# Kernel optimization log

Hardware: AMD Instinct MI355X
Metric: run time of the kernel (lower is better)

Reference implementation:

```python
import jax, jax.numpy as jnp
import numpy as np

N_NODES = 100000
N_EDGES = 1600000
H = 128
NUM_INV = 16
BN_EPS = 1e-5


def setup_inputs() -> dict:
    key = jax.random.key(0)
    ks = jax.random.split(key, 12)
    x_send = jax.random.normal(ks[0], (N_NODES, H), dtype=jnp.float32)
    x_rec = jax.random.normal(ks[1], (N_NODES, H), dtype=jnp.float32)
    index_send = jax.random.randint(ks[2], (N_EDGES,), 0, N_NODES, dtype=jnp.int32)
    index_rec = jax.random.randint(ks[3], (N_EDGES,), 0, N_NODES, dtype=jnp.int32)
    edge_attr = jax.random.normal(ks[4], (N_EDGES, NUM_INV), dtype=jnp.float32)
    d_in = 2 * H + NUM_INV
    # Linear(2H+num_inv -> H), BatchNorm1d(H) affine, Linear(H -> 1)
    W1 = jax.random.normal(ks[5], (d_in, H), dtype=jnp.float32) / np.sqrt(d_in)
    b1 = jnp.zeros((H,), dtype=jnp.float32)
    gamma = jnp.ones((H,), dtype=jnp.float32)
    beta = jnp.zeros((H,), dtype=jnp.float32)
    W_inf = jax.random.normal(ks[6], (H, 1), dtype=jnp.float32) / np.sqrt(H)
    b_inf = jnp.zeros((1,), dtype=jnp.float32)
    return {
        "x_send": x_send, "x_rec": x_rec,
        "index_send": index_send, "index_rec": index_rec,
        "edge_attr": edge_attr,
        "W1": W1, "b1": b1, "gamma": gamma, "beta": beta,
        "W_inf": W_inf, "b_inf": b_inf,
    }


def reference(x_send, x_rec, index_send, index_rec, edge_attr, W1, b1, gamma, beta, W_inf, b_inf):
    # gather sender/receiver features per edge: [E, H]
    sim_send = x_send[index_send]
    sim_rec = x_rec[index_rec]
    state = jnp.concatenate((sim_send, sim_rec, edge_attr), axis=1)  # [E, 2H+inv]
    h = state @ W1 + b1  # [E, H]
    # BatchNorm1d (training mode): batch statistics over edge dim, biased var
    mean = jnp.mean(h, axis=0)
    var = jnp.mean(jnp.square(h - mean), axis=0)
    h = (h - mean) * jax.lax.rsqrt(var + BN_EPS) * gamma + beta
    messages = jax.nn.silu(h)  # [E, H]
    edge_weights = jax.nn.sigmoid(messages @ W_inf + b_inf)  # [E, 1]
    # scatter_add over receiver index
    messages_aggr = jax.ops.segment_sum(messages * edge_weights, index_rec, num_segments=x_rec.shape[0])
    return messages_aggr
```

## Files before the change

### kernel.cpp

```cpp
#include <hip/hip_runtime.h>
#include <hip/hip_bf16.h>

#define N_NODES 100000
#define N_EDGES 1600000
#define H 128
#define NUM_INV 16
#define BN_EPS 1e-5f

typedef __attribute__((ext_vector_type(8))) short short8;
typedef __attribute__((ext_vector_type(4))) float f32x4;
typedef __attribute__((ext_vector_type(2))) float f32x2;

static __device__ __forceinline__ unsigned short f2b(float x) {
    union { float f; unsigned u; } c; c.f = x;
    unsigned r = c.u + 0x7fffu + ((c.u >> 16) & 1u);
    return (unsigned short)(r >> 16);
}
static __device__ __forceinline__ f32x2 b2f2(unsigned u) {
    union { unsigned u; float f; } lo, hi;
    lo.u = u << 16;
    hi.u = u & 0xffff0000u;
    return (f32x2){lo.f, hi.f};
}
static __device__ __forceinline__ unsigned pack2(f32x2 v) {
    return (unsigned)f2b(v.x) | ((unsigned)f2b(v.y) << 16);
}
static __device__ __forceinline__ f32x2 splat2(float s) { return (f32x2){s, s}; }

template<int CTRL, int RM>
static __device__ __forceinline__ float dppadd(float x) {
    union { float f; int i; } u, s;
    u.f = x;
    s.i = __builtin_amdgcn_update_dpp(0, u.i, CTRL, RM, 0xf, true);
    return x + s.f;
}
static __device__ __forceinline__ float wave_sum_bcast(float p) {
    p = dppadd<0x111, 0xf>(p);
    p = dppadd<0x112, 0xf>(p);
    p = dppadd<0x114, 0xf>(p);
    p = dppadd<0x118, 0xf>(p);
    p = dppadd<0x142, 0xa>(p);
    p = dppadd<0x143, 0xc>(p);
    union { float f; int i; } u, r;
    u.f = p;
    r.i = __builtin_amdgcn_readlane(u.i, 63);
    return r.f;
}

static __device__ __forceinline__ f32x2 ea_mac(const float* __restrict__ ea, int e,
                                               const f32x2* wc2, f32x2 h2) {
    const f32x4* ep = (const f32x4*)(ea + (size_t)e * NUM_INV);
    f32x4 e0 = ep[0], e1 = ep[1], e2 = ep[2], e3 = ep[3];
    float ev[16] = {e0[0],e0[1],e0[2],e0[3], e1[0],e1[1],e1[2],e1[3],
                    e2[0],e2[1],e2[2],e2[3], e3[0],e3[1],e3[2],e3[3]};
    #pragma unroll
    for (int k = 0; k < NUM_INV; ++k) h2 += splat2(ev[k]) * wc2[k];
    return h2;
}

static __device__ __forceinline__ f32x2 ea_mac_b16(const unsigned short* __restrict__ eab,
                                                   int slot, const f32x2* wc2, f32x2 h2) {
    const uint4* p = (const uint4*)(eab + (size_t)slot * NUM_INV);
    uint4 w0 = p[0], w1 = p[1];
    unsigned wv[8] = {w0.x, w0.y, w0.z, w0.w, w1.x, w1.y, w1.z, w1.w};
    #pragma unroll
    for (int k = 0; k < 8; ++k) {
        f32x2 ev = b2f2(wv[k]);
        h2 += splat2(ev.x) * wc2[2 * k] + splat2(ev.y) * wc2[2 * k + 1];
    }
    return h2;
}

__global__ void k0_wt(const float* __restrict__ W1, unsigned short* __restrict__ Wt) {
    int idx = blockIdx.x * blockDim.x + threadIdx.x;
    if (idx >= 2 * H * H) return;
    int g = idx >> 14;
    int rem = idx & 16383;
    int k = rem >> 7;
    int f = rem & 127;
    Wt[(size_t)g * H * H + (size_t)f * H + k] = f2b(W1[(size_t)(g * H + k) * H + f]);
}

__global__ __launch_bounds__(256) void k1_gemm(
    const float* __restrict__ x_send, const float* __restrict__ x_rec,
    const unsigned short* __restrict__ Wt, const float* __restrict__ b1,
    unsigned short* __restrict__ P_send, unsigned short* __restrict__ P_rec)
{
    const int g = blockIdx.y;
    const float* X = g ? x_rec : x_send;
    unsigned short* P = g ? P_rec : P_send;
    const int m0 = blockIdx.x * 32;
    const int tid = threadIdx.x;
    const int wave = tid >> 6;
    const int lane = tid & 63;
    const int quad = lane >> 4;
    const int l16 = lane & 15;
    const int n0 = wave * 32;

    const unsigned short* Wg = Wt + (size_t)g * (H * H);

    f32x4 acc[2][2];
    #pragma unroll
    for (int i = 0; i < 2; ++i)
        #pragma unroll
        for (int j = 0; j < 2; ++j)
            acc[i][j] = (f32x4){0.f, 0.f, 0.f, 0.f};

    #pragma unroll
    for (int kt = 0; kt < 4; ++kt) {
        const int kk = kt * 32;
        short8 a[2], b[2];
        #pragma unroll
        for (int ms = 0; ms < 2; ++ms) {
            const float* ap = X + (size_t)(m0 + ms * 16 + l16) * H + kk + quad * 8;
            f32x4 a0 = *(const f32x4*)ap;
            f32x4 a1 = *(const f32x4*)(ap + 4);
            short8 t;
            t[0] = (short)f2b(a0[0]); t[1] = (short)f2b(a0[1]);
            t[2] = (short)f2b(a0[2]); t[3] = (short)f2b(a0[3]);
            t[4] = (short)f2b(a1[0]); t[5] = (short)f2b(a1[1]);
            t[6] = (short)f2b(a1[2]); t[7] = (short)f2b(a1[3]);
            a[ms] = t;
        }
        #pragma unroll
        for (int ns = 0; ns < 2; ++ns)
            b[ns] = *(const short8*)(Wg + (size_t)(n0 + ns * 16 + l16) * H + kk + quad * 8);
        #pragma unroll
        for (int ms = 0; ms < 2; ++ms)
            #pragma unroll
            for (int ns = 0; ns < 2; ++ns)
                acc[ms][ns] = __builtin_amdgcn_mfma_f32_16x16x32_bf16(
                    a[ms], b[ns], acc[ms][ns], 0, 0, 0);
    }

    #pragma unroll
    for (int ms = 0; ms < 2; ++ms) {
        #pragma unroll
        for (int ns = 0; ns < 2; ++ns) {
            int col = n0 + ns * 16 + l16;
            float bias = g ? 0.f : b1[col];
            #pragma unroll
            for (int r = 0; r < 4; ++r) {
                int row = m0 + ms * 16 + quad * 4 + r;
                P[(size_t)row * H + col] = f2b(acc[ms][ns][r] + bias);
            }
        }
    }
}

__global__ void k_deg(const int* __restrict__ irec, int* __restrict__ deg) {
    int e = blockIdx.x * 256 + threadIdx.x;
    if (e < N_EDGES) atomicAdd(&deg[irec[e]], 1);
}

__global__ __launch_bounds__(512) void k_scanA(const int* __restrict__ deg, int* __restrict__ bsum) {
    __shared__ int sh[512];
    int t = threadIdx.x;
    int n = blockIdx.x * 512 + t;
    int v = (n < N_NODES) ? deg[n] : 0;
    sh[t] = v; __syncthreads();
    for (int d = 1; d < 512; d <<= 1) {
        int x = (t >= d) ? sh[t - d] : 0;
        __syncthreads();
        sh[t] += x;
        __syncthreads();
    }
    if (t == 511) bsum[blockIdx.x] = sh[511];
}

__global__ __launch_bounds__(256) void k_scanB(const int* __restrict__ bsum, int* __restrict__ bbase) {
    __shared__ int sh[256];
    int t = threadIdx.x;
    int v = (t < 196) ? bsum[t] : 0;
    sh[t] = v; __syncthreads();
    for (int d = 1; d < 256; d <<= 1) {
        int x = (t >= d) ? sh[t - d] : 0;
        __syncthreads();
        sh[t] += x;
        __syncthreads();
    }
    if (t < 196) bbase[t] = sh[t] - v;
}

__global__ __launch_bounds__(512) void k_scanC(const int* __restrict__ deg, const int* __restrict__ bbase,
                                               int* __restrict__ off, int* __restrict__ cursor) {
    __shared__ int sh[512];
    int t = threadIdx.x;
    int n = blockIdx.x * 512 + t;
    int v = (n < N_NODES) ? deg[n] : 0;
    sh[t] = v; __syncthreads();
    for (int d = 1; d < 512; d <<= 1) {
        int x = (t >= d) ? sh[t - d] : 0;
        __syncthreads();
        sh[t] += x;
        __syncthreads();
    }
    if (n < N_NODES) {
        int o = bbase[blockIdx.x] + sh[t] - v;
        off[n] = o;
        cursor[n] = o;
    }
}

__global__ void k_perm(const int* __restrict__ irec, const int* __restrict__ isend,
                       int* __restrict__ cursor,
                       int* __restrict__ perm, int* __restrict__ is_csr) {
    int e = blockIdx.x * 256 + threadIdx.x;
    if (e >= N_EDGES) return;
    int p = atomicAdd(&cursor[irec[e]], 1);
    perm[p] = e;
    is_csr[p] = isend[e];
}

__global__ __launch_bounds__(256) void k_permEA(const int* __restrict__ perm,
                                                const float* __restrict__ ea,
                                                unsigned short* __restrict__ eab)
{
    int p = blockIdx.x * 256 + threadIdx.x;
    if (p >= N_EDGES) return;
    int e = perm[p];
    const f32x4* ep = (const f32x4*)(ea + (size_t)e * NUM_INV);
    f32x4 a = ep[0], b = ep[1], c = ep[2], d = ep[3];
    unsigned o0 = pack2((f32x2){a[0], a[1]});
    unsigned o1 = pack2((f32x2){a[2], a[3]});
    unsigned o2 = pack2((f32x2){b[0], b[1]});
    unsigned o3 = pack2((f32x2){b[2], b[3]});
    unsigned o4 = pack2((f32x2){c[0], c[1]});
    unsigned o5 = pack2((f32x2){c[2], c[3]});
    unsigned o6 = pack2((f32x2){d[0], d[1]});
    unsigned o7 = pack2((f32x2){d[2], d[3]});
    uint4* op = (uint4*)(eab + (size_t)p * NUM_INV);
    op[0] = make_uint4(o0, o1, o2, o3);
    op[1] = make_uint4(o4, o5, o6, o7);
}

template<int MODE>
__global__ __launch_bounds__(256) void k2_csr(
    const unsigned short* __restrict__ Ps, const unsigned short* __restrict__ Pr,
    const int* __restrict__ is_csr, const int* __restrict__ perm,
    const float* __restrict__ ea, const unsigned short* __restrict__ eab,
    const float* __restrict__ W1,
    const int* __restrict__ off, const int* __restrict__ deg,
    float* __restrict__ stats)
{
    const int tid = threadIdx.x;
    const int wave = tid >> 6;
    const int lane = tid & 63;
    const int f0 = lane * 2;
    const float* Wc = W1 + 2 * H * H;

    f32x2 wc2[NUM_INV];
    #pragma unroll
    for (int k = 0; k < NUM_INV; ++k)
        wc2[k] = (f32x2){Wc[k * H + f0], Wc[k * H + f0 + 1]};

    int n = blockIdx.x * 4 + wave;
    int nu = __builtin_amdgcn_readfirstlane(n);
    int start = off[nu];
    int d = deg[nu];

    f32x2 pr2 = b2f2(*(const unsigned*)(Pr + (size_t)nu * H + f0));

    f32x2 s2 = {0.f, 0.f}, q2 = {0.f, 0.f};
    int i = 0;
    for (; i + 2 <= d; i += 2) {
        int is0 = __builtin_amdgcn_readfirstlane(is_csr[start + i]);
        int is1 = __builtin_amdgcn_readfirstlane(is_csr[start + i + 1]);
        unsigned ua0 = *(const unsigned*)(Ps + (size_t)is0 * H + f0);
        unsigned ua1 = *(const unsigned*)(Ps + (size_t)is1 * H + f0);
        f32x2 h0 = pr2 + b2f2(ua0);
        f32x2 h1 = pr2 + b2f2(ua1);
        if (MODE == 0) {
            h0 = ea_mac_b16(eab, start + i, wc2, h0);
            h1 = ea_mac_b16(eab, start + i + 1, wc2, h1);
        } else {
            int e0 = __builtin_amdgcn_readfirstlane(perm[start + i]);
            int e1 = __builtin_amdgcn_readfirstlane(perm[start + i + 1]);
            h0 = ea_mac(ea, e0, wc2, h0);
            h1 = ea_mac(ea, e1, wc2, h1);
        }
        s2 += h0 + h1;
        q2 += h0 * h0 + h1 * h1;
    }
    if (i < d) {
        int is0 = __builtin_amdgcn_readfirstlane(is_csr[start + i]);
        unsigned ua0 = *(const unsigned*)(Ps + (size_t)is0 * H + f0);
        f32x2 h0 = pr2 + b2f2(ua0);
        if (MODE == 0) {
            h0 = ea_mac_b16(eab, start + i, wc2, h0);
        } else {
            int e0 = __builtin_amdgcn_readfirstlane(perm[start + i]);
            h0 = ea_mac(ea, e0, wc2, h0);
        }
        s2 += h0;
        q2 += h0 * h0;
    }

    __shared__ float rs[4][128];
    __shared__ float rq[4][128];
    rs[wave][f0] = s2.x; rs[wave][f0 + 1] = s2.y;
    rq[wave][f0] = q2.x; rq[wave][f0 + 1] = q2.y;
    __syncthreads();
    if (tid < 128) {
        float ss = rs[0][tid] + rs[1][tid] + rs[2][tid] + rs[3][tid];
        float qq = rq[0][tid] + rq[1][tid] + rq[2][tid] + rq[3][tid];
        float* st = stats + (size_t)(blockIdx.x & 63) * 256;
        atomicAdd(st + tid, ss);
        atomicAdd(st + 128 + tid, qq);
    }
}

__global__ void k3_finalize(const float* __restrict__ stats,
                            const float* __restrict__ gamma, const float* __restrict__ beta,
                            float* __restrict__ ssb)
{
    int f = threadIdx.x;
    if (f >= H) return;
    float s = 0.f, q = 0.f;
    for (int b = 0; b < 64; ++b) {
        s += stats[b * 256 + f];
        q += stats[b * 256 + 128 + f];
    }
    const float invE = 1.f / (float)N_EDGES;
    float mean = s * invE;
    float var = q * invE - mean * mean;
    float scale = gamma[f] * rsqrtf(var + BN_EPS);
    ssb[f] = scale;
    ssb[H + f] = beta[f] - mean * scale;
}

__global__ __launch_bounds__(256) void k4_csr(
    const unsigned short* __restrict__ Ps, const unsigned short* __restrict__ Pr,
    const int* __restrict__ perm, const int* __restrict__ is_csr,
    const float* __restrict__ ea, const float* __restrict__ W1,
    const int* __restrict__ off, const int* __restrict__ deg,
    const float* __restrict__ ssb, const float* __restrict__ Winf,
    const float* __restrict__ binf_p, float* __restrict__ out)
{
    const int tid = threadIdx.x;
    const int wave = tid >> 6;
    const int lane = tid & 63;
    const int f0 = lane * 2;
    const float* Wc = W1 + 2 * H * H;

    f32x2 wc2[NUM_INV];
    #pragma unroll
    for (int k = 0; k < NUM_INV; ++k)
        wc2[k] = (f32x2){Wc[k * H + f0], Wc[k * H + f0 + 1]};

    int n = blockIdx.x * 4 + wave;
    int nu = __builtin_amdgcn_readfirstlane(n);
    int start = off[nu];
    int d = deg[nu];

    unsigned ub = *(const unsigned*)(Pr + (size_t)nu * H + f0);
    f32x2 pr2 = b2f2(ub);

    f32x2 sc2 = (f32x2){ssb[f0], ssb[f0 + 1]};
    f32x2 sh2 = (f32x2){ssb[H + f0], ssb[H + f0 + 1]};
    f32x2 wi2 = (f32x2){Winf[f0], Winf[f0 + 1]};
    float bi = binf_p[0];

    f32x2 a2 = {0.f, 0.f};
    int i = 0;
    for (; i + 2 <= d; i += 2) {
        int e0 = __builtin_amdgcn_readfirstlane(perm[start + i]);
        int e1 = __builtin_amdgcn_readfirstlane(perm[start + i + 1]);
        int is0 = __builtin_amdgcn_readfirstlane(is_csr[start + i]);
        int is1 = __builtin_amdgcn_readfirstlane(is_csr[start + i + 1]);
        unsigned ua0 = *(const unsigned*)(Ps + (size_t)is0 * H + f0);
        unsigned ua1 = *(const unsigned*)(Ps + (size_t)is1 * H + f0);
        f32x2 h0 = ea_mac(ea, e0, wc2, pr2 + b2f2(ua0));
        f32x2 h1 = ea_mac(ea, e1, wc2, pr2 + b2f2(ua1));
        h0 = h0 * sc2 + sh2;
        h1 = h1 * sc2 + sh2;
        float A0 = 1.f + __expf(-h0.x), B0 = 1.f + __expf(-h0.y);
        float A1 = 1.f + __expf(-h1.x), B1 = 1.f + __expf(-h1.y);
        float r0 = __builtin_amdgcn_rcpf(A0 * B0);
        float r1 = __builtin_amdgcn_rcpf(A1 * B1);
        f32x2 m0 = (f32x2){h0.x * B0 * r0, h0.y * A0 * r0};
        f32x2 m1 = (f32x2){h1.x * B1 * r1, h1.y * A1 * r1};
        f32x2 pp0 = m0 * wi2;
        f32x2 pp1 = m1 * wi2;
        float pt0 = wave_sum_bcast(pp0.x + pp0.y);
        float pt1 = wave_sum_bcast(pp1.x + pp1.y);
        float ew0 = __builtin_amdgcn_rcpf(1.f + __expf(-(pt0 + bi)));
        float ew1 = __builtin_amdgcn_rcpf(1.f + __expf(-(pt1 + bi)));
        a2 += m0 * splat2(ew0) + m1 * splat2(ew1);
    }
    if (i < d) {
        int e0 = __builtin_amdgcn_readfirstlane(perm[start + i]);
        int is0 = __builtin_amdgcn_readfirstlane(is_csr[start + i]);
        unsigned ua0 = *(const unsigned*)(Ps + (size_t)is0 * H + f0);
        f32x2 h0 = ea_mac(ea, e0, wc2, pr2 + b2f2(ua0));
        h0 = h0 * sc2 + sh2;
        float A0 = 1.f + __expf(-h0.x), B0 = 1.f + __expf(-h0.y);
        float r0 = __builtin_amdgcn_rcpf(A0 * B0);
        f32x2 m0 = (f32x2){h0.x * B0 * r0, h0.y * A0 * r0};
        f32x2 pp0 = m0 * wi2;
        float pt0 = wave_sum_bcast(pp0.x + pp0.y);
        float ew0 = __builtin_amdgcn_rcpf(1.f + __expf(-(pt0 + bi)));
        a2 += m0 * splat2(ew0);
    }
    *(float2*)(out + (size_t)nu * H + f0) = make_float2(a2.x, a2.y);
}

__global__ __launch_bounds__(256) void k4_csrB(
    const unsigned short* __restrict__ Ps, const unsigned short* __restrict__ Pr,
    const int* __restrict__ is_csr, const unsigned short* __restrict__ eab,
    const float* __restrict__ W1,
    const int* __restrict__ off, const int* __restrict__ deg,
    const float* __restrict__ ssb, const float* __restrict__ Winf,
    const float* __restrict__ binf_p, float* __restrict__ out)
{
    const int tid = threadIdx.x;
    const int wave = tid >> 6;
    const int lane = tid & 63;
    const int f0 = lane * 2;
    const float* Wc = W1 + 2 * H * H;

    f32x2 wc2[NUM_INV];
    #pragma unroll
    for (int k = 0; k < NUM_INV; ++k)
        wc2[k] = (f32x2){Wc[k * H + f0], Wc[k * H + f0 + 1]};

    int n = blockIdx.x * 4 + wave;
    int nu = __builtin_amdgcn_readfirstlane(n);
    int start = off[nu];
    int d = deg[nu];

    f32x2 pr2 = b2f2(*(const unsigned*)(Pr + (size_t)nu * H + f0));
    f32x2 sc2 = (f32x2){ssb[f0], ssb[f0 + 1]};
    f32x2 sh2 = (f32x2){ssb[H + f0], ssb[H + f0 + 1]};
    f32x2 wi2 = (f32x2){Winf[f0], Winf[f0 + 1]};
    float bi = binf_p[0];

    f32x2 a2 = {0.f, 0.f};
    int i = 0;
    for (; i + 2 <= d; i += 2) {
        int is0 = __builtin_amdgcn_readfirstlane(is_csr[start + i]);
        int is1 = __builtin_amdgcn_readfirstlane(is_csr[start + i + 1]);
        unsigned ua0 = *(const unsigned*)(Ps + (size_t)is0 * H + f0);
        unsigned ua1 = *(const unsigned*)(Ps + (size_t)is1 * H + f0);
        f32x2 h0 = ea_mac_b16(eab, start + i, wc2, pr2 + b2f2(ua0));
        f32x2 h1 = ea_mac_b16(eab, start + i + 1, wc2, pr2 + b2f2(ua1));
        h0 = h0 * sc2 + sh2;
        h1 = h1 * sc2 + sh2;
        float A0 = 1.f + __expf(-h0.x), B0 = 1.f + __expf(-h0.y);
        float A1 = 1.f + __expf(-h1.x), B1 = 1.f + __expf(-h1.y);
        float r0 = __builtin_amdgcn_rcpf(A0 * B0);
        float r1 = __builtin_amdgcn_rcpf(A1 * B1);
        f32x2 m0 = (f32x2){h0.x * B0 * r0, h0.y * A0 * r0};
        f32x2 m1 = (f32x2){h1.x * B1 * r1, h1.y * A1 * r1};
        f32x2 pp0 = m0 * wi2;
        f32x2 pp1 = m1 * wi2;
        float pt0 = wave_sum_bcast(pp0.x + pp0.y);
        float pt1 = wave_sum_bcast(pp1.x + pp1.y);
        float ew0 = __builtin_amdgcn_rcpf(1.f + __expf(-(pt0 + bi)));
        float ew1 = __builtin_amdgcn_rcpf(1.f + __expf(-(pt1 + bi)));
        a2 += m0 * splat2(ew0) + m1 * splat2(ew1);
    }
    if (i < d) {
        int is0 = __builtin_amdgcn_readfirstlane(is_csr[start + i]);
        unsigned ua0 = *(const unsigned*)(Ps + (size_t)is0 * H + f0);
        f32x2 h0 = ea_mac_b16(eab, start + i, wc2, pr2 + b2f2(ua0));
        h0 = h0 * sc2 + sh2;
        float A0 = 1.f + __expf(-h0.x), B0 = 1.f + __expf(-h0.y);
        float r0 = __builtin_amdgcn_rcpf(A0 * B0);
        f32x2 m0 = (f32x2){h0.x * B0 * r0, h0.y * A0 * r0};
        f32x2 pp0 = m0 * wi2;
        float pt0 = wave_sum_bcast(pp0.x + pp0.y);
        float ew0 = __builtin_amdgcn_rcpf(1.f + __expf(-(pt0 + bi)));
        a2 += m0 * splat2(ew0);
    }
    *(float2*)(out + (size_t)nu * H + f0) = make_float2(a2.x, a2.y);
}

extern "C" void kernel_launch(void* const* d_in, const int* in_sizes, int n_in,
                              void* d_out, int out_size, void* d_ws, size_t ws_size,
                              hipStream_t stream)
{
    const float* x_send = (const float*)d_in[0];
    const float* x_rec  = (const float*)d_in[1];
    const int*   isend  = (const int*)d_in[2];
    const int*   irec   = (const int*)d_in[3];
    const float* ea     = (const float*)d_in[4];
    const float* W1     = (const float*)d_in[5];
    const float* b1     = (const float*)d_in[6];
    const float* gamma  = (const float*)d_in[7];
    const float* beta   = (const float*)d_in[8];
    const float* Winf   = (const float*)d_in[9];
    const float* binf   = (const float*)d_in[10];
    float* out = (float*)d_out;

    char* ws = (char*)d_ws;
    unsigned short* Ps = (unsigned short*)(ws);
    unsigned short* Pr = (unsigned short*)(ws + 25600000);
    unsigned short* Wt = (unsigned short*)(ws + 51200000);
    float* stats       = (float*)(ws + 51265536);
    float* ssb         = (float*)(ws + 51331072);
    int* deg           = (int*)(ws + 51332096);
    int* off           = (int*)(ws + 51732096);
    int* cursor        = (int*)(ws + 52132096);
    int* bsum          = (int*)(ws + 52532096);
    int* bbase         = (int*)(ws + 52533120);
    int* perm          = (int*)(ws + 52534144);
    int* is_csr        = (int*)(ws + 58934144);
    unsigned short* eab = (unsigned short*)(ws + 65334272);

    const size_t WS_EAB_NEED = 116534272ULL;
    const int use_eab = (ws_size >= WS_EAB_NEED) ? 1 : 0;

    hipMemsetAsync(stats, 0, 64 * 256 * sizeof(float), stream);
    hipMemsetAsync(deg, 0, N_NODES * sizeof(int), stream);

    k0_wt<<<(2 * H * H + 255) / 256, 256, 0, stream>>>(W1, Wt);
    dim3 g1(3125, 2, 1);
    k1_gemm<<<g1, 256, 0, stream>>>(x_send, x_rec, Wt, b1, Ps, Pr);

    k_deg<<<N_EDGES / 256, 256, 0, stream>>>(irec, deg);
    k_scanA<<<196, 512, 0, stream>>>(deg, bsum);
    k_scanB<<<1, 256, 0, stream>>>(bsum, bbase);
    k_scanC<<<196, 512, 0, stream>>>(deg, bbase, off, cursor);
    k_perm<<<N_EDGES / 256, 256, 0, stream>>>(irec, isend, cursor, perm, is_csr);

    if (use_eab) {
        k_permEA<<<N_EDGES / 256, 256, 0, stream>>>(perm, ea, eab);
        k2_csr<0><<<N_NODES / 4, 256, 0, stream>>>(Ps, Pr, is_csr, perm, ea, eab, W1,
                                                   off, deg, stats);
        k3_finalize<<<1, 128, 0, stream>>>(stats, gamma, beta, ssb);
        k4_csrB<<<N_NODES / 4, 256, 0, stream>>>(Ps, Pr, is_csr, eab, W1, off, deg,
                                                 ssb, Winf, binf, out);
    } else {
        k2_csr<2><<<N_NODES / 4, 256, 0, stream>>>(Ps, Pr, is_csr, perm, ea, (const unsigned short*)0,
                                                   W1, off, deg, stats);
        k3_finalize<<<1, 128, 0, stream>>>(stats, gamma, beta, ssb);
        k4_csr<<<N_NODES / 4, 256, 0, stream>>>(Ps, Pr, perm, is_csr, ea, W1, off, deg,
                                                ssb, Winf, binf, out);
    }
}
```

Measured before the change: 846.3 us.

## Fuse edge permutation with edge-attr packing and compute edge MAC in packed fp16

Merges the CSR permutation kernel and the edge-attribute repacking kernel into one pass, so the perm array no longer has to be written and read back on the fast path. The packed edge attributes and the edge-attribute weight columns are now stored as fp16 instead of bf16, and the 16-term edge-attribute dot product runs on v_pk_fma_f16 with an fp16 accumulator in place of fp32 FMAs. Edge-attribute loads use nontemporal hints. Accumulating in fp16 lowers precision and risks error or overflow, and the scatter order now follows the write order of the fused kernel.

```diff
diff --git a/kernel.cpp b/kernel.cpp
--- a/kernel.cpp
+++ b/kernel.cpp
@@ -10,6 +10,8 @@
 typedef __attribute__((ext_vector_type(8))) short short8;
 typedef __attribute__((ext_vector_type(4))) float f32x4;
 typedef __attribute__((ext_vector_type(2))) float f32x2;
+typedef __attribute__((ext_vector_type(4))) unsigned u32x4;
+typedef _Float16 __attribute__((ext_vector_type(2))) f16x2;
 
 static __device__ __forceinline__ unsigned short f2b(float x) {
     union { float f; unsigned u; } c; c.f = x;
@@ -22,10 +24,13 @@
     hi.u = u & 0xffff0000u;
     return (f32x2){lo.f, hi.f};
 }
-static __device__ __forceinline__ unsigned pack2(f32x2 v) {
-    return (unsigned)f2b(v.x) | ((unsigned)f2b(v.y) << 16);
-}
 static __device__ __forceinline__ f32x2 splat2(float s) { return (f32x2){s, s}; }
+
+static __device__ __forceinline__ unsigned packf16(float a, float b) {
+    union { f16x2 h; unsigned u; } c;
+    c.h = (f16x2){(_Float16)a, (_Float16)b};
+    return c.u;
+}
 
 template<int CTRL, int RM>
 static __device__ __forceinline__ float dppadd(float x) {
@@ -58,16 +63,22 @@
     return h2;
 }
 
-static __device__ __forceinline__ f32x2 ea_mac_b16(const unsigned short* __restrict__ eab,
-                                                   int slot, const f32x2* wc2, f32x2 h2) {
-    const uint4* p = (const uint4*)(eab + (size_t)slot * NUM_INV);
-    uint4 w0 = p[0], w1 = p[1];
+static __device__ __forceinline__ f32x2 ea_mac_f16(const unsigned short* __restrict__ eaf,
+                                                   int slot, const unsigned* wc16, f32x2 h2) {
+    const u32x4* p = (const u32x4*)(eaf + (size_t)slot * NUM_INV);
+    u32x4 w0 = __builtin_nontemporal_load(p);
+    u32x4 w1 = __builtin_nontemporal_load(p + 1);
     unsigned wv[8] = {w0.x, w0.y, w0.z, w0.w, w1.x, w1.y, w1.z, w1.w};
+    f16x2 acc = (f16x2){(_Float16)0.f, (_Float16)0.f};
     #pragma unroll
     for (int k = 0; k < 8; ++k) {
-        f32x2 ev = b2f2(wv[k]);
-        h2 += splat2(ev.x) * wc2[2 * k] + splat2(ev.y) * wc2[2 * k + 1];
-    }
+        asm("v_pk_fma_f16 %0, %1, %2, %0 op_sel:[0,0,0] op_sel_hi:[0,1,1]"
+            : "+v"(acc) : "v"(wv[k]), "v"(wc16[2 * k]));
+        asm("v_pk_fma_f16 %0, %1, %2, %0 op_sel:[1,0,0] op_sel_hi:[1,1,1]"
+            : "+v"(acc) : "v"(wv[k]), "v"(wc16[2 * k + 1]));
+    }
+    h2.x += (float)acc.x;
+    h2.y += (float)acc.y;
     return h2;
 }
 
@@ -212,33 +223,36 @@
     is_csr[p] = isend[e];
 }
 
-__global__ __launch_bounds__(256) void k_permEA(const int* __restrict__ perm,
-                                                const float* __restrict__ ea,
-                                                unsigned short* __restrict__ eab)
-{
-    int p = blockIdx.x * 256 + threadIdx.x;
-    if (p >= N_EDGES) return;
-    int e = perm[p];
+__global__ __launch_bounds__(256) void k_permB(
+    const int* __restrict__ irec, const int* __restrict__ isend,
+    int* __restrict__ cursor, const float* __restrict__ ea,
+    int* __restrict__ is_csr, unsigned short* __restrict__ eaf)
+{
+    int e = blockIdx.x * 256 + threadIdx.x;
+    if (e >= N_EDGES) return;
+    int p = atomicAdd(&cursor[irec[e]], 1);
+    is_csr[p] = isend[e];
     const f32x4* ep = (const f32x4*)(ea + (size_t)e * NUM_INV);
     f32x4 a = ep[0], b = ep[1], c = ep[2], d = ep[3];
-    unsigned o0 = pack2((f32x2){a[0], a[1]});
-    unsigned o1 = pack2((f32x2){a[2], a[3]});
-    unsigned o2 = pack2((f32x2){b[0], b[1]});
-    unsigned o3 = pack2((f32x2){b[2], b[3]});
-    unsigned o4 = pack2((f32x2){c[0], c[1]});
-    unsigned o5 = pack2((f32x2){c[2], c[3]});
-    unsigned o6 = pack2((f32x2){d[0], d[1]});
-    unsigned o7 = pack2((f32x2){d[2], d[3]});
-    uint4* op = (uint4*)(eab + (size_t)p * NUM_INV);
-    op[0] = make_uint4(o0, o1, o2, o3);
-    op[1] = make_uint4(o4, o5, o6, o7);
+    u32x4 o0, o1;
+    o0.x = packf16(a[0], a[1]);
+    o0.y = packf16(a[2], a[3]);
+    o0.z = packf16(b[0], b[1]);
+    o0.w = packf16(b[2], b[3]);
+    o1.x = packf16(c[0], c[1]);
+    o1.y = packf16(c[2], c[3]);
+    o1.z = packf16(d[0], d[1]);
+    o1.w = packf16(d[2], d[3]);
+    u32x4* op = (u32x4*)(eaf + (size_t)p * NUM_INV);
+    op[0] = o0;
+    op[1] = o1;
 }
 
 template<int MODE>
 __global__ __launch_bounds__(256) void k2_csr(
     const unsigned short* __restrict__ Ps, const unsigned short* __restrict__ Pr,
     const int* __restrict__ is_csr, const int* __restrict__ perm,
-    const float* __restrict__ ea, const unsigned short* __restrict__ eab,
+    const float* __restrict__ ea, const unsigned short* __restrict__ eaf,
     const float* __restrict__ W1,
     const int* __restrict__ off, const int* __restrict__ deg,
     float* __restrict__ stats)
@@ -249,10 +263,17 @@
     const int f0 = lane * 2;
     const float* Wc = W1 + 2 * H * H;
 
-    f32x2 wc2[NUM_INV];
-    #pragma unroll
-    for (int k = 0; k < NUM_INV; ++k)
-        wc2[k] = (f32x2){Wc[k * H + f0], Wc[k * H + f0 + 1]};
+    f32x2 wc2[(MODE == 2) ? NUM_INV : 1];
+    unsigned wc16[(MODE == 0) ? NUM_INV : 1];
+    if (MODE == 2) {
+        #pragma unroll
+        for (int k = 0; k < NUM_INV; ++k)
+            wc2[k] = (f32x2){Wc[k * H + f0], Wc[k * H + f0 + 1]};
+    } else {
+        #pragma unroll
+        for (int k = 0; k < NUM_INV; ++k)
+            wc16[k] = packf16(Wc[k * H + f0], Wc[k * H + f0 + 1]);
+    }
 
     int n = blockIdx.x * 4 + wave;
     int nu = __builtin_amdgcn_readfirstlane(n);
@@ -271,8 +292,8 @@
         f32x2 h0 = pr2 + b2f2(ua0);
         f32x2 h1 = pr2 + b2f2(ua1);
         if (MODE == 0) {
-            h0 = ea_mac_b16(eab, start + i, wc2, h0);
-            h1 = ea_mac_b16(eab, start + i + 1, wc2, h1);
+            h0 = ea_mac_f16(eaf, start + i, wc16, h0);
+            h1 = ea_mac_f16(eaf, start + i + 1, wc16, h1);
         } else {
             int e0 = __builtin_amdgcn_readfirstlane(perm[start + i]);
             int e1 = __builtin_amdgcn_readfirstlane(perm[start + i + 1]);
@@ -287,7 +308,7 @@
         unsigned ua0 = *(const unsigned*)(Ps + (size_t)is0 * H + f0);
         f32x2 h0 = pr2 + b2f2(ua0);
         if (MODE == 0) {
-            h0 = ea_mac_b16(eab, start + i, wc2, h0);
+            h0 = ea_mac_f16(eaf, start + i, wc16, h0);
         } else {
             int e0 = __builtin_amdgcn_readfirstlane(perm[start + i]);
             h0 = ea_mac(ea, e0, wc2, h0);
@@ -407,7 +428,7 @@
 
 __global__ __launch_bounds__(256) void k4_csrB(
     const unsigned short* __restrict__ Ps, const unsigned short* __restrict__ Pr,
-    const int* __restrict__ is_csr, const unsigned short* __restrict__ eab,
+    const int* __restrict__ is_csr, const unsigned short* __restrict__ eaf,
     const float* __restrict__ W1,
     const int* __restrict__ off, const int* __restrict__ deg,
     const float* __restrict__ ssb, const float* __restrict__ Winf,
@@ -419,10 +440,10 @@
     const int f0 = lane * 2;
     const float* Wc = W1 + 2 * H * H;
 
-    f32x2 wc2[NUM_INV];
+    unsigned wc16[NUM_INV];
     #pragma unroll
     for (int k = 0; k < NUM_INV; ++k)
-        wc2[k] = (f32x2){Wc[k * H + f0], Wc[k * H + f0 + 1]};
+        wc16[k] = packf16(Wc[k * H + f0], Wc[k * H + f0 + 1]);
 
     int n = blockIdx.x * 4 + wave;
     int nu = __builtin_amdgcn_readfirstlane(n);
@@ -442,8 +463,8 @@
         int is1 = __builtin_amdgcn_readfirstlane(is_csr[start + i + 1]);
         unsigned ua0 = *(const unsigned*)(Ps + (size_t)is0 * H + f0);
         unsigned ua1 = *(const unsigned*)(Ps + (size_t)is1 * H + f0);
-        f32x2 h0 = ea_mac_b16(eab, start + i, wc2, pr2 + b2f2(ua0));
-        f32x2 h1 = ea_mac_b16(eab, start + i + 1, wc2, pr2 + b2f2(ua1));
+        f32x2 h0 = ea_mac_f16(eaf, start + i, wc16, pr2 + b2f2(ua0));
+        f32x2 h1 = ea_mac_f16(eaf, start + i + 1, wc16, pr2 + b2f2(ua1));
         h0 = h0 * sc2 + sh2;
         h1 = h1 * sc2 + sh2;
         float A0 = 1.f + __expf(-h0.x), B0 = 1.f + __expf(-h0.y);
@@ -463,7 +484,7 @@
     if (i < d) {
         int is0 = __builtin_amdgcn_readfirstlane(is_csr[start + i]);
         unsigned ua0 = *(const unsigned*)(Ps + (size_t)is0 * H + f0);
-        f32x2 h0 = ea_mac_b16(eab, start + i, wc2, pr2 + b2f2(ua0));
+        f32x2 h0 = ea_mac_f16(eaf, start + i, wc16, pr2 + b2f2(ua0));
         h0 = h0 * sc2 + sh2;
         float A0 = 1.f + __expf(-h0.x), B0 = 1.f + __expf(-h0.y);
         float r0 = __builtin_amdgcn_rcpf(A0 * B0);
@@ -506,10 +527,10 @@
     int* bbase         = (int*)(ws + 52533120);
     int* perm          = (int*)(ws + 52534144);
     int* is_csr        = (int*)(ws + 58934144);
-    unsigned short* eab = (unsigned short*)(ws + 65334272);
-
-    const size_t WS_EAB_NEED = 116534272ULL;
-    const int use_eab = (ws_size >= WS_EAB_NEED) ? 1 : 0;
+    unsigned short* eaf = (unsigned short*)(ws + 65334272);
+
+    const size_t WS_EAF_NEED = 116534272ULL;
+    const int use_eaf = (ws_size >= WS_EAF_NEED) ? 1 : 0;
 
     hipMemsetAsync(stats, 0, 64 * 256 * sizeof(float), stream);
     hipMemsetAsync(deg, 0, N_NODES * sizeof(int), stream);
@@ -522,16 +543,16 @@
     k_scanA<<<196, 512, 0, stream>>>(deg, bsum);
     k_scanB<<<1, 256, 0, stream>>>(bsum, bbase);
     k_scanC<<<196, 512, 0, stream>>>(deg, bbase, off, cursor);
-    k_perm<<<N_EDGES / 256, 256, 0, stream>>>(irec, isend, cursor, perm, is_csr);
-
-    if (use_eab) {
-        k_permEA<<<N_EDGES / 256, 256, 0, stream>>>(perm, ea, eab);
-        k2_csr<0><<<N_NODES / 4, 256, 0, stream>>>(Ps, Pr, is_csr, perm, ea, eab, W1,
+
+    if (use_eaf) {
+        k_permB<<<N_EDGES / 256, 256, 0, stream>>>(irec, isend, cursor, ea, is_csr, eaf);
+        k2_csr<0><<<N_NODES / 4, 256, 0, stream>>>(Ps, Pr, is_csr, perm, ea, eaf, W1,
                                                    off, deg, stats);
         k3_finalize<<<1, 128, 0, stream>>>(stats, gamma, beta, ssb);
-        k4_csrB<<<N_NODES / 4, 256, 0, stream>>>(Ps, Pr, is_csr, eab, W1, off, deg,
+        k4_csrB<<<N_NODES / 4, 256, 0, stream>>>(Ps, Pr, is_csr, eaf, W1, off, deg,
                                                  ssb, Winf, binf, out);
     } else {
+        k_perm<<<N_EDGES / 256, 256, 0, stream>>>(irec, isend, cursor, perm, is_csr);
         k2_csr<2><<<N_NODES / 4, 256, 0, stream>>>(Ps, Pr, is_csr, perm, ea, (const unsigned short*)0,
                                                    W1, off, deg, stats);
         k3_finalize<<<1, 128, 0, stream>>>(stats, gamma, beta, ssb);
```

Result: faster. 790.3 us (-6.6%).
